# Optimization experiments

Hardware: AMD Instinct MI355X
Metric: run time of the kernel (lower is better)

The kernel has to match this reference:

```python
import jax, jax.numpy as jnp
import numpy as np

H, DST, DCONV, EXP = 640, 16, 4, 2
DIN = H * EXP          # 1280
DTR = -(-H // 16)      # 40
EPS = 1e-6


def rmsnorm(x, w):
    rms = jnp.sqrt(jnp.mean(x * x, axis=-1, keepdims=True) + EPS)
    return x / rms * w


def bitlinear(x, w, nw):
    # RMSNorm -> ternary weight quant + int8 activation quant (STE)
    x = rmsnorm(x, nw)
    alpha = jnp.maximum(jnp.mean(jnp.abs(w)), 1e-10)
    wq = jnp.clip(jnp.round(w / alpha), -1.0, 1.0)
    wq = w + jax.lax.stop_gradient(wq - w)
    gamma = jnp.maximum(jnp.max(jnp.abs(x), axis=-1, keepdims=True), 1e-10)
    xq = jnp.clip(jnp.round(x * 127.0 / gamma), -128.0, 127.0)
    xq = x + jax.lax.stop_gradient(xq - x)
    return (xq @ wq.T) * (alpha * gamma / 127.0)


def causal_conv1d(x, cw, cb):
    # x: [B,L,D]; depthwise causal conv, kernel DCONV
    pad = DCONV - 1
    xp = jnp.pad(x, ((0, 0), (pad, 0), (0, 0)))
    L = x.shape[1]
    out = jnp.zeros_like(x)
    for k in range(DCONV):
        out = out + xp[:, pad - k:pad - k + L, :] * cw[:, k]
    return out + cb


def selective_scan(x, dt, B_mat, C_mat, A_log):
    # x,dt: [B,L,D]; B_mat,C_mat: [B,L,N]; A_log: [D,N]
    A = -jnp.exp(A_log)
    dA = jnp.exp(A[None, None] * dt[..., None])                 # [B,L,D,N]
    dBx = dt[..., None] * B_mat[:, :, None, :] * x[..., None]   # [B,L,D,N]
    dA_t = jnp.moveaxis(dA, 1, 0)
    dBx_t = jnp.moveaxis(dBx, 1, 0)
    C_t = jnp.moveaxis(C_mat, 1, 0)

    def step(h, inp):
        da, dbx, c = inp
        h = da * h + dbx
        y = jnp.sum(h * c[:, None, :], axis=-1)  # [B,D]
        return h, y

    h0 = jnp.zeros(x.shape[:1] + (x.shape[2], A_log.shape[1]), x.dtype)
    _, ys = jax.lax.scan(step, h0, (dA_t, dBx_t, C_t))
    return jnp.moveaxis(ys, 0, 1)  # [B,L,D]


def setup_inputs() -> dict:
    key = jax.random.key(0)
    ks = jax.random.split(key, 10)
    sc_in = 1.0 / np.sqrt(H)
    sc_din = 1.0 / np.sqrt(DIN)
    A = np.tile(np.arange(1, DST + 1, dtype=np.float32)[None, :], (DIN, 1))
    return {
        "x": jax.random.normal(ks[0], (2, 2048, H), jnp.float32),
        "norm_w": jnp.ones((H,), jnp.float32),
        "in_w": jax.random.normal(ks[1], (DIN * 2, H), jnp.float32) * sc_in,
        "in_nw": jnp.ones((H,), jnp.float32),
        "conv_w": jax.random.normal(ks[2], (DIN, DCONV), jnp.float32) * 0.1,
        "conv_b": jnp.zeros((DIN,), jnp.float32),
        "dtu_w": jax.random.normal(ks[3], (DTR, DIN), jnp.float32) * sc_din,
        "dtu_nw": jnp.ones((DIN,), jnp.float32),
        "dtd_w": jax.random.normal(ks[4], (DIN, DTR), jnp.float32) / np.sqrt(DTR),
        "dtd_b": jnp.zeros((DIN,), jnp.float32),
        "Bp_w": jax.random.normal(ks[5], (DST, DIN), jnp.float32) * sc_din,
        "Bp_nw": jnp.ones((DIN,), jnp.float32),
        "Cp_w": jax.random.normal(ks[6], (DST, DIN), jnp.float32) * sc_din,
        "Cp_nw": jnp.ones((DIN,), jnp.float32),
        "A_log": jnp.asarray(np.log(A)),
        "D": jnp.ones((DIN,), jnp.float32),
        "out_w": jax.random.normal(ks[7], (H, DIN), jnp.float32) * sc_din,
        "out_nw": jnp.ones((DIN,), jnp.float32),
    }


def reference(x, norm_w, in_w, in_nw, conv_w, conv_b, dtu_w, dtu_nw, dtd_w, dtd_b,
              Bp_w, Bp_nw, Cp_w, Cp_nw, A_log, D, out_w, out_nw):
    residual = x
    xn = rmsnorm(x, norm_w)
    xz = bitlinear(xn, in_w, in_nw)
    x_path, z = jnp.split(xz, 2, axis=-1)
    x_path = causal_conv1d(x_path, conv_w, conv_b)
    x_path = jax.nn.silu(x_path)
    dt = jax.nn.softplus(bitlinear(x_path, dtu_w, dtu_nw) @ dtd_w.T + dtd_b)
    B_mat = bitlinear(x_path, Bp_w, Bp_nw)
    C_mat = bitlinear(x_path, Cp_w, Cp_nw)
    y = selective_scan(x_path, dt, B_mat, C_mat, A_log)
    y = y + x_path * D
    y = y * jax.nn.silu(z)
    return bitlinear(y, out_w, out_nw) + residual
```

## Files before the change

### kernel.cpp

```cpp
#include <hip/hip_runtime.h>
#include <hip/hip_bf16.h>
#include <cmath>

#define NROWS 4096
#define H_    640
#define DIN_  1280
#define DXZ   2560
#define DTR_  40
#define DST_  16
#define LSEQ  2048
#define EPS_  1e-6f
#define NCH   64
#define CL    32
#define NDG   20
#define KSPLIT 8
#define KCH (DIN_ / KSPLIT)
#define LOG2E 1.4426950408889634f
#define RLOG2E 0.6931471805599453f

typedef __attribute__((ext_vector_type(8))) short short8;
typedef __attribute__((ext_vector_type(4))) float f32x4;
typedef __attribute__((ext_vector_type(4))) int i32x4;
typedef unsigned short ushort_t;
typedef signed char i8_t;

__device__ __forceinline__ float bf2f(short u) {
    return __uint_as_float((unsigned)(unsigned short)u << 16);
}
__device__ __forceinline__ short f2bfs(float x) { return (short)(__float_as_uint(x) >> 16); }

#define GLD16(gp, lp) __builtin_amdgcn_global_load_lds( \
    (const __attribute__((address_space(1))) unsigned int*)(unsigned long long)(gp), \
    (__attribute__((address_space(3))) unsigned int*)(unsigned int)(unsigned long long)(lp), 16, 0, 0)

__device__ __forceinline__ float wave_sum64(float v) {
    v += __shfl_xor(v, 1);  v += __shfl_xor(v, 2);  v += __shfl_xor(v, 4);
    v += __shfl_xor(v, 8);  v += __shfl_xor(v, 16); v += __shfl_xor(v, 32);
    return v;
}
__device__ __forceinline__ float wave_max64(float v) {
    v = fmaxf(v, __shfl_xor(v, 1));  v = fmaxf(v, __shfl_xor(v, 2));
    v = fmaxf(v, __shfl_xor(v, 4));  v = fmaxf(v, __shfl_xor(v, 8));
    v = fmaxf(v, __shfl_xor(v, 16)); v = fmaxf(v, __shfl_xor(v, 32));
    return v;
}
__device__ __forceinline__ float block_sum4(float v, float* red4) {
    v = wave_sum64(v);
    if ((threadIdx.x & 63) == 0) red4[threadIdx.x >> 6] = v;
    __syncthreads();
    return (red4[0] + red4[1]) + (red4[2] + red4[3]);
}
__device__ __forceinline__ float block_max4(float v, float* red4) {
    v = wave_max64(v);
    if ((threadIdx.x & 63) == 0) red4[threadIdx.x >> 6] = v;
    __syncthreads();
    return fmaxf(fmaxf(red4[0], red4[1]), fmaxf(red4[2], red4[3]));
}
__device__ __forceinline__ float block_reduce_sum256(float v, float* red) {
    int tid = threadIdx.x;
    red[tid] = v; __syncthreads();
    for (int o = 128; o; o >>= 1) { if (tid < o) red[tid] += red[tid + o]; __syncthreads(); }
    float r = red[0]; __syncthreads();
    return r;
}

__global__ __launch_bounds__(256) void k_pre(const float* __restrict__ x,
                                             const float* __restrict__ norm_w,
                                             const float* __restrict__ in_nw,
                                             const float* __restrict__ w0, const float* __restrict__ w1,
                                             const float* __restrict__ w2, const float* __restrict__ w3,
                                             const float* __restrict__ w4,
                                             int n0, int n1, int n2, int n3, int n4,
                                             i8_t* __restrict__ xq, float* __restrict__ gamma,
                                             float* __restrict__ partials,
                                             float* __restrict__ zacc ) {
    __shared__ float red[256];
    const int tid = threadIdx.x;
    if (blockIdx.x < NROWS) {
        const int r = blockIdx.x;
        const float* xr = x + (size_t)r * H_;
        const bool has2 = (tid < H_ - 512);
        float v0 = xr[tid], v1 = xr[tid + 256], v2 = has2 ? xr[tid + 512] : 0.f;
        float sum = block_sum4(v0 * v0 + v1 * v1 + v2 * v2, red);
        float r1 = 1.f / sqrtf(sum / H_ + EPS_);
        v0 *= r1 * norm_w[tid];
        v1 *= r1 * norm_w[tid + 256];
        if (has2) v2 *= r1 * norm_w[tid + 512];
        sum = block_sum4(v0 * v0 + v1 * v1 + v2 * v2, red + 4);
        float r2 = 1.f / sqrtf(sum / H_ + EPS_);
        v0 *= r2 * in_nw[tid];
        v1 *= r2 * in_nw[tid + 256];
        if (has2) v2 *= r2 * in_nw[tid + 512];
        float mx = fmaxf(fmaxf(fabsf(v0), fabsf(v1)), fabsf(v2));
        float g = fmaxf(block_max4(mx, red + 8), 1e-10f);
        if (tid == 0) gamma[r] = g;
        float s = 127.f / g;
        i8_t* o = xq + (size_t)r * H_;
        o[tid]       = (i8_t)(int)fminf(fmaxf(rintf(v0 * s), -128.f), 127.f);
        o[tid + 256] = (i8_t)(int)fminf(fmaxf(rintf(v1 * s), -128.f), 127.f);
        if (has2) o[tid + 512] = (i8_t)(int)fminf(fmaxf(rintf(v2 * s), -128.f), 127.f);
    } else {
        const int flat = blockIdx.x - NROWS;
        for (int i = flat * 256 + tid; i < NROWS * 72; i += 1280 * 256) zacc[i] = 0.f;
        const int wi = flat >> 8, xb = flat & 255;
        const float* w = (wi == 0) ? w0 : (wi == 1) ? w1 : (wi == 2) ? w2 : (wi == 3) ? w3 : w4;
        const int n = (wi == 0) ? n0 : (wi == 1) ? n1 : (wi == 2) ? n2 : (wi == 3) ? n3 : n4;
        float s = 0.f;
        for (int i = xb * 256 + tid; i < n; i += 65536) s += fabsf(w[i]);
        float t = block_reduce_sum256(s, red);
        if (tid == 0) partials[wi * 256 + xb] = t;
    }
}

__global__ __launch_bounds__(256) void k_quant_build(const float* __restrict__ in_w,
                                                     const float* __restrict__ out_w,
                                                     const float* __restrict__ dtu_w,
                                                     const float* __restrict__ Bp_w,
                                                     const float* __restrict__ Cp_w,
                                                     const float* __restrict__ partials,
                                                     float* __restrict__ alphas,
                                                     i8_t* __restrict__ q_in,
                                                     i8_t* __restrict__ q_out,
                                                     ushort_t* __restrict__ wq_sk,
                                                     int n0, int n1, int n2, int n3, int n4) {
    __shared__ double dred[256];
    const int tid = threadIdx.x;
    auto calc_alpha = [&](int wi, int n) -> float {
        double s = (double)partials[wi * 256 + tid];
        dred[tid] = s; __syncthreads();
        for (int o = 128; o; o >>= 1) { if (tid < o) dred[tid] += dred[tid + o]; __syncthreads(); }
        float a = fmaxf((float)(dred[0] / (double)n), 1e-10f);
        __syncthreads();
        return a;
    };
    if (blockIdx.x < 6400) {
        float a = calc_alpha(0, n0);
        if (blockIdx.x == 0) {
            float a1 = calc_alpha(1, n1), a2 = calc_alpha(2, n2);
            float a3 = calc_alpha(3, n3), a4 = calc_alpha(4, n4);
            if (tid == 0) {
                alphas[0] = a; alphas[1] = a1; alphas[2] = a2; alphas[3] = a3; alphas[4] = a4;
            }
        }
        int i = blockIdx.x * 256 + tid;
        q_in[i] = (i8_t)(int)fminf(fmaxf(rintf(in_w[i] / a), -1.f), 1.f);
    } else if (blockIdx.x < 9600) {
        float a = calc_alpha(4, n4);
        int i = (blockIdx.x - 6400) * 256 + tid;
        q_out[i] = (i8_t)(int)fminf(fmaxf(rintf(out_w[i] / a), -1.f), 1.f);
    } else {
        float a1 = calc_alpha(1, n1), a2 = calc_alpha(2, n2), a3 = calc_alpha(3, n3);
        int idx = (blockIdx.x - 9600) * 256 + tid;
        int t = idx / 2560, rem = idx % 2560, kb = rem / 64, l = rem % 64;
        int nloc = l & 15, kg = l >> 4;
        float alpha; const float* src; int row; bool valid = true;
        if (t < 3)      { alpha = a1; src = dtu_w; row = t * 16 + nloc; valid = (row < 40); }
        else if (t == 3){ alpha = a2; src = Bp_w;  row = nloc; }
        else            { alpha = a3; src = Cp_w;  row = nloc; }
        int k0 = kb * 32 + kg * 8;
        short8 outv;
#pragma unroll
        for (int e = 0; e < 8; ++e) {
            float q = valid ? fminf(fmaxf(rintf(src[(size_t)row * DIN_ + k0 + e] / alpha), -1.f), 1.f) : 0.f;
            outv[e] = f2bfs(q);
        }
        *(short8*)(wq_sk + (size_t)idx * 8) = outv;
    }
}

template<int BM, int BN>
__global__ __launch_bounds__(256) void k_gemm_i8(const i8_t* __restrict__ Aq,
                                                 const i8_t* __restrict__ Wq,
                                                 const float* __restrict__ alpha_p,
                                                 const float* __restrict__ gamma,
                                                 const float* __restrict__ residual,
                                                 float* __restrict__ out,
                                                 int M, int N, int K) {
    constexpr int FM = BM / 32, FN = BN / 32;
    constexpr int NL = (BM + BN) / 64;
    __shared__ i8_t As[3][BM * 64];
    __shared__ i8_t Bs[3][BN * 64];
    const int tid = threadIdx.x;
    const int w = tid >> 6, lane = tid & 63;
    const int wm = w >> 1, wn = w & 1;
    const int nwg = gridDim.x * gridDim.y;
    const int hw = blockIdx.y * gridDim.x + blockIdx.x;
    const int work = (nwg % 8 == 0) ? ((hw & 7) * (nwg >> 3) + (hw >> 3)) : hw;
    const int row0 = (work / gridDim.x) * BM;
    const int col0 = (work % gridDim.x) * BN;
    i32x4 acc[FM][FN] = {};

    auto stage = [&](int buf, int k0) {
        #pragma unroll
        for (int q = 0; q < BM / 64; ++q) {
            int c = w * BM + q * 64 + lane;
            int row = c >> 2;
            int uslot = (c & 3) ^ (row & 3);
            GLD16(Aq + (size_t)(row0 + row) * K + k0 + uslot * 16,
                  (char*)As[buf] + (w * BM + q * 64) * 16);
        }
        #pragma unroll
        for (int q = 0; q < BN / 64; ++q) {
            int c = w * BN + q * 64 + lane;
            int row = c >> 2;
            int uslot = (c & 3) ^ (row & 3);
            GLD16(Wq + (size_t)(col0 + row) * K + k0 + uslot * 16,
                  (char*)Bs[buf] + (w * BN + q * 64) * 16);
        }
    };

    const int NT = K >> 6;
    stage(0, 0);
    if (NT > 1) stage(1, 64);
    int cur = 0;
    for (int t = 0; t < NT; ++t) {
        if (t + 2 < NT) {
            int nb = cur + 2; if (nb >= 3) nb -= 3;
            stage(nb, (t + 2) << 6);
            if constexpr (NL == 2)      asm volatile("s_waitcnt vmcnt(4)" ::: "memory");
            else if constexpr (NL == 3) asm volatile("s_waitcnt vmcnt(6)" ::: "memory");
            else                        asm volatile("s_waitcnt vmcnt(8)" ::: "memory");
        } else if (t + 1 < NT) {
            if constexpr (NL == 2)      asm volatile("s_waitcnt vmcnt(2)" ::: "memory");
            else if constexpr (NL == 3) asm volatile("s_waitcnt vmcnt(3)" ::: "memory");
            else                        asm volatile("s_waitcnt vmcnt(4)" ::: "memory");
        } else {
            asm volatile("s_waitcnt vmcnt(0)" ::: "memory");
        }
        __builtin_amdgcn_s_barrier();

        i32x4 a[FM], b[FN];
        #pragma unroll
        for (int i = 0; i < FM; ++i) {
            int row = wm * (BM / 2) + i * 16 + (lane & 15);
            int byt = row * 64 + (((lane >> 4) ^ (row & 3)) << 4);
            a[i] = *(const i32x4*)((const char*)As[cur] + byt);
        }
        #pragma unroll
        for (int j = 0; j < FN; ++j) {
            int row = wn * (BN / 2) + j * 16 + (lane & 15);
            int byt = row * 64 + (((lane >> 4) ^ (row & 3)) << 4);
            b[j] = *(const i32x4*)((const char*)Bs[cur] + byt);
        }
        #pragma unroll
        for (int i = 0; i < FM; ++i)
            #pragma unroll
            for (int j = 0; j < FN; ++j)
                acc[i][j] = __builtin_amdgcn_mfma_i32_16x16x64_i8(a[i], b[j], acc[i][j], 0, 0, 0);
        asm volatile("" ::: "memory");
        __builtin_amdgcn_s_barrier();
        ++cur; if (cur == 3) cur = 0;
    }

    const float alpha = alpha_p[0];
    #pragma unroll
    for (int i = 0; i < FM; ++i) {
        #pragma unroll
        for (int r = 0; r < 4; ++r) {
            int row = row0 + wm * (BM / 2) + i * 16 + (lane >> 4) * 4 + r;
            float s = alpha * gamma[row] * (1.f / 127.f);
            #pragma unroll
            for (int j = 0; j < FN; ++j) {
                int col = col0 + wn * (BN / 2) + j * 16 + (lane & 15);
                float o = (float)acc[i][j][r] * s;
                if (residual) o += residual[(size_t)row * N + col];
                out[(size_t)row * N + col] = o;
            }
        }
    }
}

__global__ __launch_bounds__(256) void k_conv_norm(const float* __restrict__ xz,
                                                   const float* __restrict__ cw, const float* __restrict__ cb,
                                                   const float* __restrict__ dtu_nw,
                                                   const float* __restrict__ Bp_nw,
                                                   const float* __restrict__ Cp_nw,
                                                   float* __restrict__ xp,
                                                   float* __restrict__ rinv_out, float* __restrict__ g3) {
    const int bb = blockIdx.x;
    const int row = ((bb & 7) << 9) | (bb >> 3);
    const int tid = threadIdx.x;
    const int l = row & (LSEQ - 1);
    __shared__ float red4[16];
    float vv[5];
    float ss = 0.f;
#pragma unroll
    for (int j = 0; j < 5; ++j) {
        int d = tid + j * 256;
        f32x4 c4 = *(const f32x4*)(cw + (size_t)d * 4);
        const float* base = xz + (size_t)row * DXZ + d;
        float s = cb[d] + base[0] * c4[0];
        if (l >= 1) s += base[-(ptrdiff_t)DXZ] * c4[1];
        if (l >= 2) s += base[-(ptrdiff_t)(2 * DXZ)] * c4[2];
        if (l >= 3) s += base[-(ptrdiff_t)(3 * DXZ)] * c4[3];
        float v = s / (1.f + __builtin_amdgcn_exp2f(-s * LOG2E));
        vv[j] = v;
        ss += v * v;
        xp[(size_t)row * DIN_ + d] = v;
    }
    float sum = block_sum4(ss, red4);
    float rms = 1.f / sqrtf(sum / DIN_ + EPS_);
    float m0 = 0.f, m1 = 0.f, m2 = 0.f;
#pragma unroll
    for (int j = 0; j < 5; ++j) {
        int d = tid + j * 256;
        float t = vv[j] * rms;
        m0 = fmaxf(m0, fabsf(t * dtu_nw[d]));
        m1 = fmaxf(m1, fabsf(t * Bp_nw[d]));
        m2 = fmaxf(m2, fabsf(t * Cp_nw[d]));
    }
    float g0 = block_max4(m0, red4 + 4);
    float g1 = block_max4(m1, red4 + 8);
    float g2 = block_max4(m2, red4 + 12);
    if (tid == 0) {
        rinv_out[row]       = rms;
        g3[row]             = fmaxf(g0, 1e-10f);
        g3[NROWS + row]     = fmaxf(g1, 1e-10f);
        g3[2 * NROWS + row] = fmaxf(g2, 1e-10f);
    }
}

__global__ __launch_bounds__(256) void k_skinny_mfma(const float* __restrict__ xp,
                                                     const float* __restrict__ rinv,
                                                     const float* __restrict__ dtu_nw,
                                                     const float* __restrict__ Bp_nw,
                                                     const float* __restrict__ Cp_nw,
                                                     const float* __restrict__ g3,
                                                     const ushort_t* __restrict__ wq_sk,
                                                     float* __restrict__ dtu_acc,
                                                     float* __restrict__ B_acc,
                                                     float* __restrict__ C_acc) {
    const int tid = threadIdx.x;
    const int w = tid >> 6, l = tid & 63;
    const int row0 = blockIdx.x * 64;
    const int kc0 = blockIdx.y * KCH;
    __shared__ float s_xp[64 * 36];
    __shared__ float s_nw[3 * KCH];
    for (int i = tid; i < 3 * KCH; i += 256) {
        int m = i / KCH, j = i - m * KCH;
        const float* nw = (m == 0) ? dtu_nw : (m == 1) ? Bp_nw : Cp_nw;
        s_nw[i] = nw[kc0 + j];
    }
    const int arow = row0 + w * 16 + (l & 15);
    const float ri = rinv[arow];
    const float s0 = 127.f / g3[arow];
    const float s1 = 127.f / g3[NROWS + arow];
    const float s2 = 127.f / g3[2 * NROWS + arow];
    const int kgrp = l >> 4;
    f32x4 acc[5] = {};

    for (int ks = 0; ks < KCH / 32; ++ks) {
        const int kc = kc0 + ks * 32;
        __syncthreads();
        {
            int srow = tid >> 2, scol = (tid & 3) * 8;
            const float* gp = xp + (size_t)(row0 + srow) * DIN_ + kc + scol;
            f32x4 u0 = *(const f32x4*)gp;
            f32x4 u1 = *(const f32x4*)(gp + 4);
            *(f32x4*)(s_xp + srow * 36 + scol)     = u0;
            *(f32x4*)(s_xp + srow * 36 + scol + 4) = u1;
        }
        __syncthreads();
        const float* sp = s_xp + (w * 16 + (l & 15)) * 36 + kgrp * 8;
        f32x4 t0 = *(const f32x4*)sp;
        f32x4 t1 = *(const f32x4*)(sp + 4);
        float t[8] = { t0[0]*ri, t0[1]*ri, t0[2]*ri, t0[3]*ri,
                       t1[0]*ri, t1[1]*ri, t1[2]*ri, t1[3]*ri };
        short8 a0, a1, a2;
        #pragma unroll
        for (int e = 0; e < 8; ++e) {
            int kk = ks * 32 + kgrp * 8 + e;
            float q0 = fminf(fmaxf(rintf(t[e] * s_nw[kk]           * s0), -128.f), 127.f);
            float q1 = fminf(fmaxf(rintf(t[e] * s_nw[KCH + kk]     * s1), -128.f), 127.f);
            float q2 = fminf(fmaxf(rintf(t[e] * s_nw[2 * KCH + kk] * s2), -128.f), 127.f);
            a0[e] = f2bfs(q0); a1[e] = f2bfs(q1); a2[e] = f2bfs(q2);
        }
        const int kbg = kc >> 5;
        short8 b0 = *(const short8*)(wq_sk + ((size_t)(0 * 40 + kbg) * 64 + l) * 8);
        short8 b1 = *(const short8*)(wq_sk + ((size_t)(1 * 40 + kbg) * 64 + l) * 8);
        short8 b2 = *(const short8*)(wq_sk + ((size_t)(2 * 40 + kbg) * 64 + l) * 8);
        short8 b3 = *(const short8*)(wq_sk + ((size_t)(3 * 40 + kbg) * 64 + l) * 8);
        short8 b4 = *(const short8*)(wq_sk + ((size_t)(4 * 40 + kbg) * 64 + l) * 8);
        acc[0] = __builtin_amdgcn_mfma_f32_16x16x32_bf16(a0, b0, acc[0], 0, 0, 0);
        acc[1] = __builtin_amdgcn_mfma_f32_16x16x32_bf16(a0, b1, acc[1], 0, 0, 0);
        acc[2] = __builtin_amdgcn_mfma_f32_16x16x32_bf16(a0, b2, acc[2], 0, 0, 0);
        acc[3] = __builtin_amdgcn_mfma_f32_16x16x32_bf16(a1, b3, acc[3], 0, 0, 0);
        acc[4] = __builtin_amdgcn_mfma_f32_16x16x32_bf16(a2, b4, acc[4], 0, 0, 0);
    }

    const int col = l & 15;
    const int rbase = row0 + w * 16 + (l >> 4) * 4;
    #pragma unroll
    for (int j = 0; j < 4; ++j) {
        int r = rbase + j;
        atomicAdd(&dtu_acc[(size_t)r * DTR_ + col],      acc[0][j]);
        atomicAdd(&dtu_acc[(size_t)r * DTR_ + 16 + col], acc[1][j]);
        if (col < 8) atomicAdd(&dtu_acc[(size_t)r * DTR_ + 32 + col], acc[2][j]);
        atomicAdd(&B_acc[(size_t)r * DST_ + col], acc[3][j]);
        atomicAdd(&C_acc[(size_t)r * DST_ + col], acc[4][j]);
    }
}

__global__ __launch_bounds__(256) void k_dtd(const float* __restrict__ U,
                                             const float* __restrict__ W,
                                             const float* __restrict__ bias,
                                             const float* __restrict__ g3,
                                             const float* __restrict__ alphas,
                                             float* __restrict__ dt) {
    const int c0 = blockIdx.x * 64;
    const int r0 = blockIdx.y * 32;
    const int tid = threadIdx.x;
    const int col = tid & 63, rg = tid >> 6;
    __shared__ float s_w[64 * 41];
    __shared__ float s_u[32 * 40];
    for (int i = tid; i < 64 * 40; i += 256) {
        int cc = i / 40, t = i - cc * 40;
        s_w[cc * 41 + t] = W[(size_t)c0 * 40 + i];
    }
    const float alpha = alphas[1];
    for (int i = tid; i < 32 * 40; i += 256) {
        int rr = i / 40;
        s_u[i] = ((U[(size_t)r0 * 40 + i] * alpha) * g3[r0 + rr]) * (1.f / 127.f);
    }
    __syncthreads();
    float w[40];
#pragma unroll
    for (int t = 0; t < 40; t++) w[t] = s_w[col * 41 + t];
    const float b = bias[c0 + col];
    for (int r8 = 0; r8 < 8; ++r8) {
        const int row = rg * 8 + r8;
        const float* ur = s_u + row * 40;
        float a0 = b, a1 = 0.f, a2 = 0.f, a3 = 0.f;
#pragma unroll
        for (int t = 0; t < 40; t += 4) {
            f32x4 uv = *(const f32x4*)(ur + t);
            a0 = fmaf(uv[0], w[t],     a0);
            a1 = fmaf(uv[1], w[t + 1], a1);
            a2 = fmaf(uv[2], w[t + 2], a2);
            a3 = fmaf(uv[3], w[t + 3], a3);
        }
        float s = (a0 + a1) + (a2 + a3);
        float e = __builtin_amdgcn_exp2f(-fabsf(s) * LOG2E);
        float sp = fmaxf(s, 0.f) + __builtin_amdgcn_logf(1.f + e) * RLOG2E;
        dt[(size_t)(r0 + row) * DIN_ + c0 + col] = sp;
    }
}

__global__ __launch_bounds__(256) void k_scan_a(const float* __restrict__ dt, const float* __restrict__ xp,
                                                const float* __restrict__ Bm, const float* __restrict__ A_log,
                                                const float* __restrict__ g3, const float* __restrict__ alphas,
                                                float* __restrict__ hloc, float* __restrict__ sdt_out) {
    const int tid = threadIdx.x;
    const int q = tid & 3, dloc = tid >> 2;
    const int dg = blockIdx.x, c = blockIdx.y, b = blockIdx.z;
    const int d = dg * 64 + dloc;
    const int l0 = c * CL;
    __shared__ float s_B[CL * 16];
    if (tid < CL * 4) {
        int rg = b * LSEQ + l0 + (tid >> 2);
        float a2 = alphas[2];
        float gB = g3[NROWS + rg];
        f32x4 Bv = *(const f32x4*)(Bm + (size_t)rg * DST_ + (tid & 3) * 4);
        f32x4 o;
#pragma unroll
        for (int k = 0; k < 4; ++k) o[k] = ((Bv[k] * a2) * gB) * (1.f / 127.f);
        *(f32x4*)(s_B + tid * 4) = o;
    }
    f32x4 Av = *(const f32x4*)(A_log + (size_t)d * DST_ + q * 4);
    float A2[4];
#pragma unroll
    for (int j = 0; j < 4; ++j) A2[j] = -expf(Av[j]) * LOG2E;
    __syncthreads();
    const float* dtp = dt + (size_t)(b * LSEQ + l0) * DIN_ + d;
    const float* xpp = xp + (size_t)(b * LSEQ + l0) * DIN_ + d;
    float h[4] = {};
    float sdt = 0.f;
    float dtv = *dtp, xv = *xpp;
    for (int l = 0; l < CL; ++l) {
        float ndt = 0.f, nx = 0.f;
        if (l + 1 < CL) { ndt = dtp[(size_t)(l + 1) * DIN_]; nx = xpp[(size_t)(l + 1) * DIN_]; }
        f32x4 Bv = *(const f32x4*)(s_B + l * 16 + q * 4);
        float dtx = dtv * xv;
        sdt += dtv;
#pragma unroll
        for (int j = 0; j < 4; ++j) {
            float dA = __builtin_amdgcn_exp2f(A2[j] * dtv);
            h[j] = fmaf(dA, h[j], Bv[j] * dtx);
        }
        dtv = ndt; xv = nx;
    }
    size_t base = ((size_t)(b * NDG + dg) * 64 + c) * 1024 + tid * 4;
    *(f32x4*)(hloc + base) = (f32x4){h[0], h[1], h[2], h[3]};
    if (q == 0) sdt_out[((size_t)(b * NDG + dg) * 64 + c) * 64 + dloc] = sdt;
}

__global__ __launch_bounds__(256) void k_scan_b(float* __restrict__ hloc, const float* __restrict__ sdt,
                                                const float* __restrict__ A_log) {
    const int tid = threadIdx.x;
    const int idx = blockIdx.x;
    const int b = idx / (NDG * 64);
    const int rem = idx % (NDG * 64);
    const int dg = rem / 64, dloc = rem % 64;
    const int d = dg * 64 + dloc;
    __shared__ float s_h[64 * 17];
    __shared__ float s_sdt[64];
    __shared__ float s_A2[16];
    const size_t gb = (size_t)(b * NDG + dg) * 64;
#pragma unroll
    for (int i = 0; i < 4; ++i) {
        int c = i * 16 + (tid >> 4), n = tid & 15;
        s_h[c * 17 + n] = hloc[(gb + c) * 1024 + dloc * 16 + n];
    }
    if (tid < 64) s_sdt[tid] = sdt[(gb + tid) * 64 + dloc];
    else if (tid < 80) s_A2[tid - 64] = -expf(A_log[(size_t)d * DST_ + (tid - 64)]) * LOG2E;
    __syncthreads();
    const int w = tid >> 6, lane = tid & 63;
#pragma unroll
    for (int nn = 0; nn < 4; ++nn) {
        int n = w * 4 + nn;
        float h = s_h[lane * 17 + n];
        float P = __builtin_amdgcn_exp2f(s_A2[n] * s_sdt[lane]);
#pragma unroll
        for (int s = 1; s < 64; s <<= 1) {
            float hp = __shfl_up(h, s);
            float Pp = __shfl_up(P, s);
            if (lane >= s) { h = fmaf(P, hp, h); P *= Pp; }
        }
        float Hi = __shfl_up(h, 1);
        if (lane == 0) Hi = 0.f;
        s_h[lane * 17 + n] = Hi;
    }
    __syncthreads();
#pragma unroll
    for (int i = 0; i < 4; ++i) {
        int c = i * 16 + (tid >> 4), n = tid & 15;
        hloc[(gb + c) * 1024 + dloc * 16 + n] = s_h[c * 17 + n];
    }
}

__global__ __launch_bounds__(256) void k_scan_c(const float* __restrict__ dt, const float* __restrict__ xp,
                                                const float* __restrict__ Bm, const float* __restrict__ Cm,
                                                const float* __restrict__ xz, const float* __restrict__ A_log,
                                                const float* __restrict__ Dvec, const float* __restrict__ g3,
                                                const float* __restrict__ alphas,
                                                const float* __restrict__ Hinit, float* __restrict__ y) {
    const int tid = threadIdx.x;
    const int q = tid & 3, dloc = tid >> 2;
    const int dg = blockIdx.x, c = blockIdx.y, b = blockIdx.z;
    const int d = dg * 64 + dloc;
    const int l0 = c * CL;
    __shared__ float s_B[CL * 16], s_C[CL * 16];
    if (tid < CL * 4) {
        int rg = b * LSEQ + l0 + (tid >> 2);
        float a2 = alphas[2];
        float gB = g3[NROWS + rg];
        f32x4 Bv = *(const f32x4*)(Bm + (size_t)rg * DST_ + (tid & 3) * 4);
        f32x4 o;
#pragma unroll
        for (int k = 0; k < 4; ++k) o[k] = ((Bv[k] * a2) * gB) * (1.f / 127.f);
        *(f32x4*)(s_B + tid * 4) = o;
    } else {
        int t2 = tid - CL * 4;
        int rg = b * LSEQ + l0 + (t2 >> 2);
        float a3 = alphas[3];
        float gC = g3[2 * NROWS + rg];
        f32x4 Cv = *(const f32x4*)(Cm + (size_t)rg * DST_ + (t2 & 3) * 4);
        f32x4 o;
#pragma unroll
        for (int k = 0; k < 4; ++k) o[k] = ((Cv[k] * a3) * gC) * (1.f / 127.f);
        *(f32x4*)(s_C + t2 * 4) = o;
    }
    f32x4 Av = *(const f32x4*)(A_log + (size_t)d * DST_ + q * 4);
    float A2[4];
#pragma unroll
    for (int j = 0; j < 4; ++j) A2[j] = -expf(Av[j]) * LOG2E;
    const float Dd = Dvec[d];
    __syncthreads();
    const float* dtp = dt + (size_t)(b * LSEQ + l0) * DIN_ + d;
    const float* xpp = xp + (size_t)(b * LSEQ + l0) * DIN_ + d;
    const float* zp  = xz + (size_t)(b * LSEQ + l0) * DXZ + DIN_ + d;
    float* yp = y + (size_t)(b * LSEQ + l0) * DIN_ + d;
    size_t base = ((size_t)(b * NDG + dg) * 64 + c) * 1024 + tid * 4;
    f32x4 hv = *(const f32x4*)(Hinit + base);
    float h[4] = {hv[0], hv[1], hv[2], hv[3]};
    float dtv = *dtp, xv = *xpp, zv = *zp;
    for (int l = 0; l < CL; ++l) {
        float ndt = 0.f, nx = 0.f, nz = 0.f;
        if (l + 1 < CL) {
            ndt = dtp[(size_t)(l + 1) * DIN_];
            nx  = xpp[(size_t)(l + 1) * DIN_];
            nz  = zp[(size_t)(l + 1) * DXZ];
        }
        f32x4 Bv = *(const f32x4*)(s_B + l * 16 + q * 4);
        f32x4 Cv = *(const f32x4*)(s_C + l * 16 + q * 4);
        float dtx = dtv * xv;
        float yv = 0.f;
#pragma unroll
        for (int j = 0; j < 4; ++j) {
            float dA = __builtin_amdgcn_exp2f(A2[j] * dtv);
            h[j] = fmaf(dA, h[j], Bv[j] * dtx);
            yv = fmaf(h[j], Cv[j], yv);
        }
        yv += __shfl_xor(yv, 1);
        yv += __shfl_xor(yv, 2);
        if (q == 0) {
            float sig = 1.f / (1.f + __builtin_amdgcn_exp2f(-zv * LOG2E));
            yp[(size_t)l * DIN_] = (yv + xv * Dd) * (zv * sig);
        }
        dtv = ndt; xv = nx; zv = nz;
    }
}

__global__ __launch_bounds__(256) void k_norm_y(const float* __restrict__ y,
                                                const float* __restrict__ out_nw,
                                                i8_t* __restrict__ yq, float* __restrict__ gy) {
    const int r = blockIdx.x, tid = threadIdx.x;
    const float* yr = y + (size_t)r * DIN_;
    __shared__ float red4[8];
    float v[5];
    float ss = 0.f;
#pragma unroll
    for (int j = 0; j < 5; j++) { v[j] = yr[tid + j * 256]; ss += v[j] * v[j]; }
    float sum = block_sum4(ss, red4);
    float rms = 1.f / sqrtf(sum / DIN_ + EPS_);
    float mx = 0.f;
#pragma unroll
    for (int j = 0; j < 5; j++) {
        int i = tid + j * 256;
        v[j] = v[j] * rms * out_nw[i];
        mx = fmaxf(mx, fabsf(v[j]));
    }
    float g = fmaxf(block_max4(mx, red4 + 4), 1e-10f);
    if (tid == 0) gy[r] = g;
    float s = 127.f / g;
#pragma unroll
    for (int j = 0; j < 5; j++) {
        int i = tid + j * 256;
        yq[(size_t)r * DIN_ + i] = (i8_t)(int)fminf(fmaxf(rintf(v[j] * s), -128.f), 127.f);
    }
}

extern "C" void kernel_launch(void* const* d_in, const int* in_sizes, int n_in,
                              void* d_out, int out_size, void* d_ws, size_t ws_size,
                              hipStream_t stream) {
    (void)in_sizes; (void)n_in; (void)out_size;
    const float* x      = (const float*)d_in[0];
    const float* norm_w = (const float*)d_in[1];
    const float* in_w   = (const float*)d_in[2];
    const float* in_nw  = (const float*)d_in[3];
    const float* conv_w = (const float*)d_in[4];
    const float* conv_b = (const float*)d_in[5];
    const float* dtu_w  = (const float*)d_in[6];
    const float* dtu_nw = (const float*)d_in[7];
    const float* dtd_w  = (const float*)d_in[8];
    const float* dtd_b  = (const float*)d_in[9];
    const float* Bp_w   = (const float*)d_in[10];
    const float* Bp_nw  = (const float*)d_in[11];
    const float* Cp_w   = (const float*)d_in[12];
    const float* Cp_nw  = (const float*)d_in[13];
    const float* A_log  = (const float*)d_in[14];
    const float* Dv     = (const float*)d_in[15];
    const float* out_w  = (const float*)d_in[16];
    const float* out_nw = (const float*)d_in[17];

    float* ws = (float*)d_ws;
    float* alphas   = ws;
    float* partials = ws + 8;
    float* xq1      = ws + 8 + 5 * 256;
    float* gamma1   = xq1 + (size_t)NROWS * H_;
    float* xz       = gamma1 + NROWS;
    float* xp       = xz + (size_t)NROWS * DXZ;
    float* xpn     = xp + (size_t)NROWS * DIN_;
    float* g3       = xpn + (size_t)NROWS * DIN_;
    float* dtu_out  = g3 + 3 * NROWS;
    float* Bmat     = dtu_out + (size_t)NROWS * DTR_;
    float* Cmat     = Bmat + (size_t)NROWS * DST_;
    float* dtb      = Cmat + (size_t)NROWS * DST_;
    float* gy       = dtb + (size_t)NROWS * DIN_;
    float* wq_in    = gy + NROWS;
    float* wq_dtu   = wq_in + (size_t)DXZ * H_;
    float* wq_Bp    = wq_dtu + (size_t)DTR_ * DIN_;
    float* wq_Cp    = wq_Bp + (size_t)DST_ * DIN_;
    float* wq_out   = wq_Cp + (size_t)DST_ * DIN_;
    float* rinv     = wq_out + (size_t)H_ * DIN_;
    float* wq_sk    = rinv + NROWS;
    float* sdt      = wq_sk + 51200;
    size_t need = (size_t)((sdt + 2 * NDG * 64 * 64) - ws) * sizeof(float);
    if (ws_size < need) return;

    float* hloc = xq1;

    const int n0 = DXZ * H_, n1 = DTR_ * DIN_, n2 = DST_ * DIN_, n3 = DST_ * DIN_, n4 = H_ * DIN_;
    hipLaunchKernelGGL(k_pre, dim3(NROWS + 5 * 256), dim3(256), 0, stream,
                       x, norm_w, in_nw, in_w, dtu_w, Bp_w, Cp_w, out_w,
                       n0, n1, n2, n3, n4, (i8_t*)xq1, gamma1, partials, dtu_out);
    hipLaunchKernelGGL(k_quant_build, dim3(9650), dim3(256), 0, stream,
                       in_w, out_w, dtu_w, Bp_w, Cp_w, partials, alphas,
                       (i8_t*)wq_in, (i8_t*)wq_out, (ushort_t*)wq_sk,
                       n0, n1, n2, n3, n4);

    hipLaunchKernelGGL((k_gemm_i8<128, 128>), dim3(DXZ / 128, NROWS / 128), dim3(256), 0, stream,
                       (const i8_t*)xq1, (const i8_t*)wq_in, alphas + 0, gamma1,
                       (const float*)nullptr, xz, NROWS, DXZ, H_);
    hipLaunchKernelGGL(k_conv_norm, dim3(NROWS), dim3(256), 0, stream,
                       xz, conv_w, conv_b, dtu_nw, Bp_nw, Cp_nw, xp, rinv, g3);
    hipLaunchKernelGGL(k_skinny_mfma, dim3(NROWS / 64, KSPLIT), dim3(256), 0, stream,
                       xp, rinv, dtu_nw, Bp_nw, Cp_nw, g3, (const ushort_t*)wq_sk,
                       dtu_out, Bmat, Cmat);
    hipLaunchKernelGGL(k_dtd, dim3(DIN_ / 64, NROWS / 32), dim3(256), 0, stream,
                       dtu_out, dtd_w, dtd_b, g3, alphas, dtb);

    hipLaunchKernelGGL(k_scan_a, dim3(NDG, NCH, 2), dim3(256), 0, stream,
                       dtb, xp, Bmat, A_log, g3, alphas, hloc, sdt);
    hipLaunchKernelGGL(k_scan_b, dim3(2 * NDG * 64), dim3(256), 0, stream, hloc, sdt, A_log);
    hipLaunchKernelGGL(k_scan_c, dim3(NDG, NCH, 2), dim3(256), 0, stream,
                       dtb, xp, Bmat, Cmat, xz, A_log, Dv, g3, alphas, hloc, xpn );

    hipLaunchKernelGGL(k_norm_y, dim3(NROWS), dim3(256), 0, stream, xpn , out_nw,
                       (i8_t*)dtb , gy);
    hipLaunchKernelGGL((k_gemm_i8<64, 64>), dim3(H_ / 64, NROWS / 64), dim3(256), 0, stream,
                       (const i8_t*)dtb , (const i8_t*)wq_out, alphas + 4, gy,
                       x , (float*)d_out, NROWS, H_, DIN_);
}
```

Baseline: 200.1 us.

## Store dt as bf16 and compute chunk dt sums in the dt kernel

```diff
diff --git a/kernel.cpp b/kernel.cpp
--- a/kernel.cpp
+++ b/kernel.cpp
@@ -28,6 +28,10 @@
     return __uint_as_float((unsigned)(unsigned short)u << 16);
 }
 __device__ __forceinline__ short f2bfs(float x) { return (short)(__float_as_uint(x) >> 16); }
+__device__ __forceinline__ ushort_t f2bf_rne(float x) {
+    __hip_bfloat16 h = __float2bfloat16(x);
+    return *(ushort_t*)&h;
+}
 
 #define GLD16(gp, lp) __builtin_amdgcn_global_load_lds( \
     (const __attribute__((address_space(1))) unsigned int*)(unsigned long long)(gp), \
@@ -406,13 +410,15 @@
                                              const float* __restrict__ bias,
                                              const float* __restrict__ g3,
                                              const float* __restrict__ alphas,
-                                             float* __restrict__ dt) {
+                                             ushort_t* __restrict__ dt,
+                                             float* __restrict__ sdt_out) {
     const int c0 = blockIdx.x * 64;
     const int r0 = blockIdx.y * 32;
     const int tid = threadIdx.x;
     const int col = tid & 63, rg = tid >> 6;
     __shared__ float s_w[64 * 41];
     __shared__ float s_u[32 * 40];
+    __shared__ float s_red[64 * 4];
     for (int i = tid; i < 64 * 40; i += 256) {
         int cc = i / 40, t = i - cc * 40;
         s_w[cc * 41 + t] = W[(size_t)c0 * 40 + i];
@@ -427,6 +433,7 @@
 #pragma unroll
     for (int t = 0; t < 40; t++) w[t] = s_w[col * 41 + t];
     const float b = bias[c0 + col];
+    float part = 0.f;
     for (int r8 = 0; r8 < 8; ++r8) {
         const int row = rg * 8 + r8;
         const float* ur = s_u + row * 40;
@@ -442,14 +449,23 @@
         float s = (a0 + a1) + (a2 + a3);
         float e = __builtin_amdgcn_exp2f(-fabsf(s) * LOG2E);
         float sp = fmaxf(s, 0.f) + __builtin_amdgcn_logf(1.f + e) * RLOG2E;
-        dt[(size_t)(r0 + row) * DIN_ + c0 + col] = sp;
-    }
-}
-
-__global__ __launch_bounds__(256) void k_scan_a(const float* __restrict__ dt, const float* __restrict__ xp,
+        ushort_t spb = f2bf_rne(sp);
+        dt[(size_t)(r0 + row) * DIN_ + c0 + col] = spb;
+        part += bf2f((short)spb);
+    }
+    s_red[col * 4 + rg] = part;
+    __syncthreads();
+    if (tid < 64) {
+        float sdt = (s_red[tid * 4] + s_red[tid * 4 + 1]) + (s_red[tid * 4 + 2] + s_red[tid * 4 + 3]);
+        int bb = blockIdx.y >> 6, cc = blockIdx.y & 63;
+        sdt_out[(((size_t)(bb * NDG + blockIdx.x)) * 64 + cc) * 64 + tid] = sdt;
+    }
+}
+
+__global__ __launch_bounds__(256) void k_scan_a(const ushort_t* __restrict__ dt, const float* __restrict__ xp,
                                                 const float* __restrict__ Bm, const float* __restrict__ A_log,
                                                 const float* __restrict__ g3, const float* __restrict__ alphas,
-                                                float* __restrict__ hloc, float* __restrict__ sdt_out) {
+                                                float* __restrict__ hloc) {
     const int tid = threadIdx.x;
     const int q = tid & 3, dloc = tid >> 2;
     const int dg = blockIdx.x, c = blockIdx.y, b = blockIdx.z;
@@ -471,17 +487,15 @@
 #pragma unroll
     for (int j = 0; j < 4; ++j) A2[j] = -expf(Av[j]) * LOG2E;
     __syncthreads();
-    const float* dtp = dt + (size_t)(b * LSEQ + l0) * DIN_ + d;
+    const ushort_t* dtp = dt + (size_t)(b * LSEQ + l0) * DIN_ + d;
     const float* xpp = xp + (size_t)(b * LSEQ + l0) * DIN_ + d;
     float h[4] = {};
-    float sdt = 0.f;
-    float dtv = *dtp, xv = *xpp;
+    float dtv = bf2f((short)*dtp), xv = *xpp;
     for (int l = 0; l < CL; ++l) {
         float ndt = 0.f, nx = 0.f;
-        if (l + 1 < CL) { ndt = dtp[(size_t)(l + 1) * DIN_]; nx = xpp[(size_t)(l + 1) * DIN_]; }
+        if (l + 1 < CL) { ndt = bf2f((short)dtp[(size_t)(l + 1) * DIN_]); nx = xpp[(size_t)(l + 1) * DIN_]; }
         f32x4 Bv = *(const f32x4*)(s_B + l * 16 + q * 4);
         float dtx = dtv * xv;
-        sdt += dtv;
 #pragma unroll
         for (int j = 0; j < 4; ++j) {
             float dA = __builtin_amdgcn_exp2f(A2[j] * dtv);
@@ -491,7 +505,6 @@
     }
     size_t base = ((size_t)(b * NDG + dg) * 64 + c) * 1024 + tid * 4;
     *(f32x4*)(hloc + base) = (f32x4){h[0], h[1], h[2], h[3]};
-    if (q == 0) sdt_out[((size_t)(b * NDG + dg) * 64 + c) * 64 + dloc] = sdt;
 }
 
 __global__ __launch_bounds__(256) void k_scan_b(float* __restrict__ hloc, const float* __restrict__ sdt,
@@ -538,7 +551,7 @@
     }
 }
 
-__global__ __launch_bounds__(256) void k_scan_c(const float* __restrict__ dt, const float* __restrict__ xp,
+__global__ __launch_bounds__(256) void k_scan_c(const ushort_t* __restrict__ dt, const float* __restrict__ xp,
                                                 const float* __restrict__ Bm, const float* __restrict__ Cm,
                                                 const float* __restrict__ xz, const float* __restrict__ A_log,
                                                 const float* __restrict__ Dvec, const float* __restrict__ g3,
@@ -576,18 +589,18 @@
     for (int j = 0; j < 4; ++j) A2[j] = -expf(Av[j]) * LOG2E;
     const float Dd = Dvec[d];
     __syncthreads();
-    const float* dtp = dt + (size_t)(b * LSEQ + l0) * DIN_ + d;
+    const ushort_t* dtp = dt + (size_t)(b * LSEQ + l0) * DIN_ + d;
     const float* xpp = xp + (size_t)(b * LSEQ + l0) * DIN_ + d;
     const float* zp  = xz + (size_t)(b * LSEQ + l0) * DXZ + DIN_ + d;
     float* yp = y + (size_t)(b * LSEQ + l0) * DIN_ + d;
     size_t base = ((size_t)(b * NDG + dg) * 64 + c) * 1024 + tid * 4;
     f32x4 hv = *(const f32x4*)(Hinit + base);
     float h[4] = {hv[0], hv[1], hv[2], hv[3]};
-    float dtv = *dtp, xv = *xpp, zv = *zp;
+    float dtv = bf2f((short)*dtp), xv = *xpp, zv = *zp;
     for (int l = 0; l < CL; ++l) {
         float ndt = 0.f, nx = 0.f, nz = 0.f;
         if (l + 1 < CL) {
-            ndt = dtp[(size_t)(l + 1) * DIN_];
+            ndt = bf2f((short)dtp[(size_t)(l + 1) * DIN_]);
             nx  = xpp[(size_t)(l + 1) * DIN_];
             nz  = zp[(size_t)(l + 1) * DXZ];
         }
@@ -708,13 +721,14 @@
                        xp, rinv, dtu_nw, Bp_nw, Cp_nw, g3, (const ushort_t*)wq_sk,
                        dtu_out, Bmat, Cmat);
     hipLaunchKernelGGL(k_dtd, dim3(DIN_ / 64, NROWS / 32), dim3(256), 0, stream,
-                       dtu_out, dtd_w, dtd_b, g3, alphas, dtb);
+                       dtu_out, dtd_w, dtd_b, g3, alphas, (ushort_t*)dtb, sdt);
 
     hipLaunchKernelGGL(k_scan_a, dim3(NDG, NCH, 2), dim3(256), 0, stream,
-                       dtb, xp, Bmat, A_log, g3, alphas, hloc, sdt);
+                       (const ushort_t*)dtb, xp, Bmat, A_log, g3, alphas, hloc);
     hipLaunchKernelGGL(k_scan_b, dim3(2 * NDG * 64), dim3(256), 0, stream, hloc, sdt, A_log);
     hipLaunchKernelGGL(k_scan_c, dim3(NDG, NCH, 2), dim3(256), 0, stream,
-                       dtb, xp, Bmat, Cmat, xz, A_log, Dv, g3, alphas, hloc, xpn );
+                       (const ushort_t*)dtb, xp, Bmat, Cmat, xz, A_log, Dv, g3, alphas,
+                       hloc, xpn );
 
     hipLaunchKernelGGL(k_norm_y, dim3(NROWS), dim3(256), 0, stream, xpn , out_nw,
                        (i8_t*)dtb , gy);
```

Result: slower. 206.3 us (+3.1%).
